# Optimization experiments

Measured on AMD Instinct MI355X. Metric: run time of the kernel, lower is better.

Reference implementation:

```python
import jax, jax.numpy as jnp
import numpy as np

N_NODES = 50000
TAU = 1.0 + (1.0 / 1000.0) * (0.1 - 1.0)  # anneal step 1 -> 0.9991


def setup_inputs() -> dict:
    key = jax.random.key(0)
    ks = jax.random.split(key, 8)
    N, F, H, E, K = N_NODES, 128, 128, 800000, 5
    node_features = jax.random.normal(ks[0], (N, F), dtype=jnp.float32)
    src = jnp.sort(jax.random.randint(ks[1], (E,), 0, N, dtype=jnp.int32))
    dst = jax.random.randint(ks[2], (E,), 0, N, dtype=jnp.int32)
    u_noise = jax.random.uniform(ks[3], (K, E), dtype=jnp.float32,
                                 minval=1e-6, maxval=1.0 - 1e-6)
    # MLP params: Linear(2F -> H), ReLU, Linear(H -> 1)
    W1 = jax.random.normal(ks[4], (2 * F, H), dtype=jnp.float32) / np.sqrt(2 * F)
    b1 = jnp.zeros((H,), dtype=jnp.float32)
    W2 = jax.random.normal(ks[5], (H, 1), dtype=jnp.float32) / np.sqrt(H)
    b2 = jnp.zeros((1,), dtype=jnp.float32)
    return {"node_features": node_features, "W1": W1, "b1": b1,
            "W2": W2, "b2": b2, "u_noise": u_noise, "src": src, "dst": dst}


def reference(node_features, W1, b1, W2, b2, u_noise, src, dst):
    N = N_NODES
    F = node_features.shape[1]
    # per-edge MLP on concat([x_u, x_v]) without materializing the (E, 2F) concat
    x_u = node_features[src]                      # (E, F)
    x_v = node_features[dst]                      # (E, F)
    h = jax.nn.relu(x_u @ W1[:F] + x_v @ W1[F:] + b1)   # (E, H)
    z = (h @ W2 + b2)[:, 0]                       # (E,)
    # per-node (segment) log-softmax over each node's neighbor edges
    zmax = jax.ops.segment_max(z, src, num_segments=N)
    ze = z - zmax[src]
    denom = jax.ops.segment_sum(jnp.exp(ze), src, num_segments=N)
    log_pi = ze - jnp.log(denom)[src]             # (E,)
    # k rounds of Gumbel-softmax sampling
    g = -jnp.log(-jnp.log(u_noise))               # (K, E)
    scores = (log_pi[None, :] + g) / TAU          # (K, E)

    def seg_softmax(s):
        m = jax.ops.segment_max(s, src, num_segments=N)
        e = jnp.exp(s - m[src])
        return e / jax.ops.segment_sum(e, src, num_segments=N)[src]

    def seg_argmax_dst(s):
        m = jax.ops.segment_max(s, src, num_segments=N)
        hit = s >= m[src]
        sel = jax.ops.segment_max(jnp.where(hit, dst, -1), src, num_segments=N)
        return sel  # (N,) selected neighbor per node, per round

    soft = jax.vmap(seg_softmax)(scores)          # (K, E) gumbel-softmax probs
    selected = jax.vmap(seg_argmax_dst)(scores)   # (K, N) sampled neighbor ids
    return selected, soft
```

## Files before the change

kernel.cpp:

```cpp
#include <hip/hip_runtime.h>

#define FEAT 128
#define HID  128
#define XS_S 132
#define MAXE 768
#define AS_S 132

__global__ __launch_bounds__(256) void gemm_ab(
    const float* __restrict__ X, const float* __restrict__ W1,
    const float* __restrict__ b1, float* __restrict__ A,
    float* __restrict__ B, int N) {
  __shared__ float xs[32 * XS_S];
  __shared__ float ws[32 * 64];
  const int t = threadIdx.x;
  const int n0 = blockIdx.x * 128;
  const int j0 = blockIdx.y * 64;
  const bool isA = j0 < 128;
  const float* Wbase = W1 + (isA ? j0 : 128 * HID + (j0 - 128));
  float* Obase = isA ? (A + j0) : (B + (j0 - 128));

  const int tn = t & 31;
  const int tc = t >> 5;

  float acc[4][8];
#pragma unroll
  for (int rr = 0; rr < 4; ++rr)
#pragma unroll
    for (int c = 0; c < 8; ++c) acc[rr][c] = 0.f;

  const int ln = t >> 3;
  const int lf = (t & 7) * 4;

  for (int kc = 0; kc < 4; ++kc) {
    __syncthreads();
#pragma unroll
    for (int rep = 0; rep < 4; ++rep) {
      const int nl = ln + rep * 32;
      const int n = n0 + nl;
      float4 v = make_float4(0.f, 0.f, 0.f, 0.f);
      if (n < N) v = *(const float4*)(X + (size_t)n * FEAT + kc * 32 + lf);
      xs[(lf + 0) * XS_S + nl] = v.x;
      xs[(lf + 1) * XS_S + nl] = v.y;
      xs[(lf + 2) * XS_S + nl] = v.z;
      xs[(lf + 3) * XS_S + nl] = v.w;
    }
#pragma unroll
    for (int rep = 0; rep < 2; ++rep) {
      const int idx = rep * 256 + t;
      const int wr = idx >> 4;
      const int c4 = (idx & 15) * 4;
      *(float4*)&ws[wr * 64 + c4] =
          *(const float4*)(Wbase + (size_t)(kc * 32 + wr) * HID + c4);
    }
    __syncthreads();

#pragma unroll 8
    for (int k = 0; k < 32; ++k) {
      const float4 xv = *(const float4*)&xs[k * XS_S + tn * 4];
      const float4 w0 = *(const float4*)&ws[k * 64 + tc * 8];
      const float4 w1 = *(const float4*)&ws[k * 64 + tc * 8 + 4];
      const float xr[4] = {xv.x, xv.y, xv.z, xv.w};
#pragma unroll
      for (int rr = 0; rr < 4; ++rr) {
        acc[rr][0] = fmaf(xr[rr], w0.x, acc[rr][0]);
        acc[rr][1] = fmaf(xr[rr], w0.y, acc[rr][1]);
        acc[rr][2] = fmaf(xr[rr], w0.z, acc[rr][2]);
        acc[rr][3] = fmaf(xr[rr], w0.w, acc[rr][3]);
        acc[rr][4] = fmaf(xr[rr], w1.x, acc[rr][4]);
        acc[rr][5] = fmaf(xr[rr], w1.y, acc[rr][5]);
        acc[rr][6] = fmaf(xr[rr], w1.z, acc[rr][6]);
        acc[rr][7] = fmaf(xr[rr], w1.w, acc[rr][7]);
      }
    }
  }

  float bb[8];
#pragma unroll
  for (int c = 0; c < 8; ++c) bb[c] = 0.f;
  if (isA) {
    *(float4*)&bb[0] = *(const float4*)(b1 + j0 + tc * 8);
    *(float4*)&bb[4] = *(const float4*)(b1 + j0 + tc * 8 + 4);
  }
#pragma unroll
  for (int rr = 0; rr < 4; ++rr) {
    const int n = n0 + tn * 4 + rr;
    if (n < N) {
      float* o = Obase + (size_t)n * HID + tc * 8;
      *(float4*)o = make_float4(acc[rr][0] + bb[0], acc[rr][1] + bb[1],
                                acc[rr][2] + bb[2], acc[rr][3] + bb[3]);
      *(float4*)(o + 4) = make_float4(acc[rr][4] + bb[4], acc[rr][5] + bb[5],
                                      acc[rr][6] + bb[6], acc[rr][7] + bb[7]);
    }
  }
}

__global__ __launch_bounds__(256) void fused_edge_seg(
    const float* __restrict__ A, const float* __restrict__ B,
    const float* __restrict__ W2, const float* __restrict__ b2,
    const int* __restrict__ src, const int* __restrict__ dst,
    const float* __restrict__ U, float* __restrict__ out_sel,
    float* __restrict__ out_soft, int N, int E, int K) {
  __shared__ float zs[MAXE];
  __shared__ int srcs[MAXE];
  __shared__ int dsts[MAXE];
  __shared__ float as[16 * AS_S];
  __shared__ int rsl[17];
  const int t = threadIdx.x;
  const int n0 = blockIdx.x * 16;
  const float INVTAU = 1.0f / 0.9991f;

  if (t < 17) {
    const int n = min(n0 + t, N);
    int lo = 0, hi = E;
    while (lo < hi) {
      const int mid = (lo + hi) >> 1;
      if (src[mid] < n) lo = mid + 1; else hi = mid;
    }
    rsl[t] = lo;
  }
#pragma unroll
  for (int rep = 0; rep < 2; ++rep) {
    const int idx = rep * 256 + t;
    const int row = idx >> 5;
    const int q4 = (idx & 31) * 4;
    const int gn = n0 + row;
    float4 v = make_float4(0.f, 0.f, 0.f, 0.f);
    if (gn < N) v = *(const float4*)(A + (size_t)gn * HID + q4);
    *(float4*)&as[row * AS_S + q4] = v;
  }
  __syncthreads();
  const int e_lo = rsl[0];
  const int cnt = min(rsl[16] - e_lo, MAXE);

  for (int i = t; i < cnt; i += 256) {
    srcs[i] = src[e_lo + i];
    dsts[i] = dst[e_lo + i];
  }
  __syncthreads();

  if (cnt > 0) {
    const int g2 = (t >> 4) * 2;
    const int l = t & 15;
    const float4 w0 = *(const float4*)(W2 + l * 8);
    const float4 w1 = *(const float4*)(W2 + l * 8 + 4);
    const float bias2 = b2[0];

#define LOADB(base_, B00, B01, B10, B11)                                      \
    {                                                                         \
      const int c0 = min((base_) + g2, cnt - 1);                              \
      const int c1 = min((base_) + g2 + 1, cnt - 1);                          \
      const float4* Bv0 = (const float4*)(B + (size_t)dsts[c0] * HID) + l * 2;\
      const float4* Bv1 = (const float4*)(B + (size_t)dsts[c1] * HID) + l * 2;\
      B00 = Bv0[0]; B01 = Bv0[1]; B10 = Bv1[0]; B11 = Bv1[1];                 \
    }

#define COMPUTE(base_, B00, B01, B10, B11)                                    \
    {                                                                         \
      const int i0 = (base_) + g2;                                            \
      const int c0 = min(i0, cnt - 1);                                        \
      const int c1 = min(i0 + 1, cnt - 1);                                    \
      const int u0 = srcs[c0] - n0;                                           \
      const int u1 = srcs[c1] - n0;                                           \
      const float4 a00 = *(const float4*)&as[u0 * AS_S + l * 8];              \
      const float4 a01 = *(const float4*)&as[u0 * AS_S + l * 8 + 4];          \
      const float4 a10 = *(const float4*)&as[u1 * AS_S + l * 8];              \
      const float4 a11 = *(const float4*)&as[u1 * AS_S + l * 8 + 4];          \
      float p0 = fmaxf(a00.x + B00.x, 0.f) * w0.x                             \
               + fmaxf(a00.y + B00.y, 0.f) * w0.y                             \
               + fmaxf(a00.z + B00.z, 0.f) * w0.z                             \
               + fmaxf(a00.w + B00.w, 0.f) * w0.w                             \
               + fmaxf(a01.x + B01.x, 0.f) * w1.x                             \
               + fmaxf(a01.y + B01.y, 0.f) * w1.y                             \
               + fmaxf(a01.z + B01.z, 0.f) * w1.z                             \
               + fmaxf(a01.w + B01.w, 0.f) * w1.w;                            \
      float p1 = fmaxf(a10.x + B10.x, 0.f) * w0.x                             \
               + fmaxf(a10.y + B10.y, 0.f) * w0.y                             \
               + fmaxf(a10.z + B10.z, 0.f) * w0.z                             \
               + fmaxf(a10.w + B10.w, 0.f) * w0.w                             \
               + fmaxf(a11.x + B11.x, 0.f) * w1.x                             \
               + fmaxf(a11.y + B11.y, 0.f) * w1.y                             \
               + fmaxf(a11.z + B11.z, 0.f) * w1.z                             \
               + fmaxf(a11.w + B11.w, 0.f) * w1.w;                            \
      _Pragma("unroll")                                                       \
      for (int m = 8; m >= 1; m >>= 1) {                                      \
        p0 += __shfl_xor(p0, m);                                              \
        p1 += __shfl_xor(p1, m);                                              \
      }                                                                       \
      if (l == 0) {                                                           \
        if (i0 < cnt) zs[i0] = p0 + bias2;                                    \
        if (i0 + 1 < cnt) zs[i0 + 1] = p1 + bias2;                            \
      }                                                                       \
    }

    float4 xb0, xb1, xb2, xb3;
    float4 yb0, yb1, yb2, yb3;
    LOADB(0, xb0, xb1, xb2, xb3)
    for (int base = 0; base < cnt; base += 64) {
      LOADB(base + 32, yb0, yb1, yb2, yb3)
      COMPUTE(base, xb0, xb1, xb2, xb3)
      LOADB(base + 64, xb0, xb1, xb2, xb3)
      COMPUTE(base + 32, yb0, yb1, yb2, yb3)
    }
#undef LOADB
#undef COMPUTE
  }
  __syncthreads();

  const int lane = t & 63;
  const int qtr = lane >> 4;
  const int ql = lane & 15;
  const int li = (t >> 6) * 4 + qtr;
  const int n = n0 + li;

  int start = 0, deg = 0;
  if (n < N) { start = rsl[li]; deg = rsl[li + 1] - start; }

  if (__all(deg <= 32)) {
    if (n >= N) return;
    if (deg == 0) {
      if (ql == 0)
        for (int k = 0; k < K; ++k) out_sel[(size_t)k * N + n] = -2147483648.0f;
      return;
    }
    const bool a0 = 2 * ql < deg;
    const bool a1 = 2 * ql + 1 < deg;
    const int le0 = start - e_lo + 2 * ql;
    const int le1 = le0 + 1;
    const int e0 = start + 2 * ql;
    const int e1 = e0 + 1;
    const float z0 = a0 ? zs[le0] : -INFINITY;
    const float z1 = a1 ? zs[le1] : -INFINITY;
    const int d0 = a0 ? dsts[le0] : -1;
    const int d1 = a1 ? dsts[le1] : -1;

    float zmax = fmaxf(z0, z1);
#pragma unroll
    for (int m = 8; m >= 1; m >>= 1) zmax = fmaxf(zmax, __shfl_xor(zmax, m));
    float den = (a0 ? __expf(z0 - zmax) : 0.f) + (a1 ? __expf(z1 - zmax) : 0.f);
#pragma unroll
    for (int m = 8; m >= 1; m >>= 1) den += __shfl_xor(den, m);
    const float logd = __logf(den);
    const float lp0 = (z0 - zmax) - logd;
    const float lp1 = (z1 - zmax) - logd;

    if (K == 5) {
      const size_t ce0 = (size_t)min(e0, E - 1);
      const size_t ce1 = (size_t)min(e1, E - 1);
      float u00, u01, u02, u03, u04, u10, u11, u12, u13, u14;
      u00 = U[0 * (size_t)E + ce0]; u10 = U[0 * (size_t)E + ce1];
      u01 = U[1 * (size_t)E + ce0]; u11 = U[1 * (size_t)E + ce1];
      u02 = U[2 * (size_t)E + ce0]; u12 = U[2 * (size_t)E + ce1];
      u03 = U[3 * (size_t)E + ce0]; u13 = U[3 * (size_t)E + ce1];
      u04 = U[4 * (size_t)E + ce0]; u14 = U[4 * (size_t)E + ce1];

#define GUMEX0(u) (a0 ? __expf((lp0 - __logf(-__logf(u))) * INVTAU) : 0.f)
#define GUMEX1(u) (a1 ? __expf((lp1 - __logf(-__logf(u))) * INVTAU) : 0.f)
      const float x00 = GUMEX0(u00), x10 = GUMEX1(u10);
      const float x01 = GUMEX0(u01), x11 = GUMEX1(u11);
      const float x02 = GUMEX0(u02), x12 = GUMEX1(u12);
      const float x03 = GUMEX0(u03), x13 = GUMEX1(u13);
      const float x04 = GUMEX0(u04), x14 = GUMEX1(u14);
#undef GUMEX0
#undef GUMEX1

#define ROUND(kk, ex0, ex1)                                                   \
      {                                                                       \
        float d2 = (ex0) + (ex1);                                             \
        float mx;                                                             \
        int md;                                                               \
        if ((ex1) > (ex0))      { mx = (ex1); md = d1; }                      \
        else if ((ex1) < (ex0)) { mx = (ex0); md = d0; }                      \
        else                    { mx = (ex0); md = max(d0, d1); }             \
        _Pragma("unroll")                                                     \
        for (int m = 8; m >= 1; m >>= 1) {                                    \
          d2 += __shfl_xor(d2, m);                                            \
          const float ox = __shfl_xor(mx, m);                                 \
          const int od = __shfl_xor(md, m);                                   \
          if (ox > mx) { mx = ox; md = od; }                                  \
          else if (ox == mx) md = max(md, od);                                \
        }                                                                     \
        if (ql == 0) out_sel[(size_t)(kk) * N + n] = (float)md;               \
        const float inv = __builtin_amdgcn_rcpf(d2);                          \
        if (a0) out_soft[(size_t)(kk) * E + e0] = (ex0) * inv;                \
        if (a1) out_soft[(size_t)(kk) * E + e1] = (ex1) * inv;                \
      }
      ROUND(0, x00, x10)
      ROUND(1, x01, x11)
      ROUND(2, x02, x12)
      ROUND(3, x03, x13)
      ROUND(4, x04, x14)
#undef ROUND
      return;
    }

    for (int k = 0; k < K; ++k) {
      float ex0 = 0.f, ex1 = 0.f;
      if (a0) {
        const float uu = U[(size_t)k * E + e0];
        const float gum = -__logf(-__logf(uu));
        ex0 = __expf((lp0 + gum) * INVTAU);
      }
      if (a1) {
        const float uu = U[(size_t)k * E + e1];
        const float gum = -__logf(-__logf(uu));
        ex1 = __expf((lp1 + gum) * INVTAU);
      }
      float d2 = ex0 + ex1;
      float mx;
      int md;
      if (ex1 > ex0)      { mx = ex1; md = d1; }
      else if (ex1 < ex0) { mx = ex0; md = d0; }
      else                { mx = ex0; md = max(d0, d1); }
#pragma unroll
      for (int m = 8; m >= 1; m >>= 1) {
        d2 += __shfl_xor(d2, m);
        const float ox = __shfl_xor(mx, m);
        const int od = __shfl_xor(md, m);
        if (ox > mx) { mx = ox; md = od; }
        else if (ox == mx) md = max(md, od);
      }
      if (ql == 0) out_sel[(size_t)k * N + n] = (float)md;
      const float inv = __builtin_amdgcn_rcpf(d2);
      if (a0) out_soft[(size_t)k * E + e0] = ex0 * inv;
      if (a1) out_soft[(size_t)k * E + e1] = ex1 * inv;
    }
    return;
  }

  const int lbase = (t >> 6) * 4;
  for (int j = 0; j < 4; ++j) {
    const int lj = lbase + j;
    const int nn = n0 + lj;
    if (nn >= N) continue;
    const int st = rsl[lj];
    const int dg = rsl[lj + 1] - st;
    const int lst = st - e_lo;
    if (dg == 0) {
      if (lane == 0)
        for (int k = 0; k < K; ++k) out_sel[(size_t)k * N + nn] = -2147483648.0f;
      continue;
    }
    float zmax = -INFINITY;
    for (int c = lane; c < dg; c += 64) zmax = fmaxf(zmax, zs[lst + c]);
#pragma unroll
    for (int m = 32; m >= 1; m >>= 1) zmax = fmaxf(zmax, __shfl_xor(zmax, m));
    float den = 0.f;
    for (int c = lane; c < dg; c += 64) den += expf(zs[lst + c] - zmax);
#pragma unroll
    for (int m = 32; m >= 1; m >>= 1) den += __shfl_xor(den, m);
    const float logd = logf(den);

    for (int k = 0; k < K; ++k) {
      float m2 = -INFINITY;
      for (int c = lane; c < dg; c += 64) {
        const float gum = -logf(-logf(U[(size_t)k * E + st + c]));
        const float s = ((zs[lst + c] - zmax) - logd + gum) * INVTAU;
        m2 = fmaxf(m2, s);
      }
#pragma unroll
      for (int m = 32; m >= 1; m >>= 1) m2 = fmaxf(m2, __shfl_xor(m2, m));
      float d2 = 0.f;
      int cand = -1;
      for (int c = lane; c < dg; c += 64) {
        const float gum = -logf(-logf(U[(size_t)k * E + st + c]));
        const float s = ((zs[lst + c] - zmax) - logd + gum) * INVTAU;
        d2 += expf(s - m2);
        if (s >= m2) cand = max(cand, dsts[lst + c]);
      }
#pragma unroll
      for (int m = 32; m >= 1; m >>= 1) d2 += __shfl_xor(d2, m);
#pragma unroll
      for (int m = 32; m >= 1; m >>= 1) cand = max(cand, __shfl_xor(cand, m));
      if (lane == 0) out_sel[(size_t)k * N + nn] = (float)cand;
      for (int c = lane; c < dg; c += 64) {
        const float gum = -logf(-logf(U[(size_t)k * E + st + c]));
        const float s = ((zs[lst + c] - zmax) - logd + gum) * INVTAU;
        out_soft[(size_t)k * E + st + c] = expf(s - m2) / d2;
      }
    }
  }
}

extern "C" void kernel_launch(void* const* d_in, const int* in_sizes, int n_in,
                              void* d_out, int out_size, void* d_ws, size_t ws_size,
                              hipStream_t stream) {
  const float* X  = (const float*)d_in[0];
  const float* W1 = (const float*)d_in[1];
  const float* b1 = (const float*)d_in[2];
  const float* W2 = (const float*)d_in[3];
  const float* b2 = (const float*)d_in[4];
  const float* U  = (const float*)d_in[5];
  const int* src  = (const int*)d_in[6];
  const int* dst  = (const int*)d_in[7];
  const int E = in_sizes[6];
  const int K = in_sizes[5] / E;
  const int N = in_sizes[0] / FEAT;

  float* A = (float*)d_ws;
  float* B = A + (size_t)N * HID;

  float* out_sel  = (float*)d_out;
  float* out_soft = (float*)d_out + (size_t)K * N;

  hipLaunchKernelGGL(gemm_ab, dim3((N + 127) / 128, 4), dim3(256), 0, stream,
                     X, W1, b1, A, B, N);
  hipLaunchKernelGGL(fused_edge_seg, dim3((N + 15) / 16), dim3(256), 0, stream,
                     A, B, W2, b2, src, dst, U, out_sel, out_soft, N, E, K);
}
```

Before: 232.1 us.

## Stage per-edge Gumbel exponentials in shared memory with block-wide coalesced passes

Replaces the per-node lane mapping, which used two edges per lane with a 64-lane fallback for high-degree nodes, with a uniform scheme. Log-probabilities are first written to shared memory. Then, for each round, all 256 threads compute exp-Gumbel values for the block's edge range with coalesced noise loads. Each 16-lane group then reduces its node's edges from shared memory to get the softmax sum and argmax. This removes the divergent fallback path and the uncoalesced noise reads, but adds block barriers per round and reuses shared buffers (srcs, as) as scratch.

```diff
diff --git a/kernel.cpp b/kernel.cpp
--- a/kernel.cpp
+++ b/kernel.cpp
@@ -206,6 +206,9 @@
   }
   __syncthreads();
 
+  float* lps = (float*)srcs;
+  float* exs = as;
+
   const int lane = t & 63;
   const int qtr = lane >> 4;
   const int ql = lane & 15;
@@ -214,170 +217,55 @@
 
   int start = 0, deg = 0;
   if (n < N) { start = rsl[li]; deg = rsl[li + 1] - start; }
-
-  if (__all(deg <= 32)) {
-    if (n >= N) return;
-    if (deg == 0) {
-      if (ql == 0)
-        for (int k = 0; k < K; ++k) out_sel[(size_t)k * N + n] = -2147483648.0f;
-      return;
-    }
-    const bool a0 = 2 * ql < deg;
-    const bool a1 = 2 * ql + 1 < deg;
-    const int le0 = start - e_lo + 2 * ql;
-    const int le1 = le0 + 1;
-    const int e0 = start + 2 * ql;
-    const int e1 = e0 + 1;
-    const float z0 = a0 ? zs[le0] : -INFINITY;
-    const float z1 = a1 ? zs[le1] : -INFINITY;
-    const int d0 = a0 ? dsts[le0] : -1;
-    const int d1 = a1 ? dsts[le1] : -1;
-
-    float zmax = fmaxf(z0, z1);
+  const int lst = start - e_lo;
+
+  {
+    float zmax = -INFINITY;
+    for (int c = ql; c < deg; c += 16) zmax = fmaxf(zmax, zs[lst + c]);
 #pragma unroll
     for (int m = 8; m >= 1; m >>= 1) zmax = fmaxf(zmax, __shfl_xor(zmax, m));
-    float den = (a0 ? __expf(z0 - zmax) : 0.f) + (a1 ? __expf(z1 - zmax) : 0.f);
+    float den = 0.f;
+    for (int c = ql; c < deg; c += 16) den += __expf(zs[lst + c] - zmax);
 #pragma unroll
     for (int m = 8; m >= 1; m >>= 1) den += __shfl_xor(den, m);
     const float logd = __logf(den);
-    const float lp0 = (z0 - zmax) - logd;
-    const float lp1 = (z1 - zmax) - logd;
-
-    if (K == 5) {
-      const size_t ce0 = (size_t)min(e0, E - 1);
-      const size_t ce1 = (size_t)min(e1, E - 1);
-      float u00, u01, u02, u03, u04, u10, u11, u12, u13, u14;
-      u00 = U[0 * (size_t)E + ce0]; u10 = U[0 * (size_t)E + ce1];
-      u01 = U[1 * (size_t)E + ce0]; u11 = U[1 * (size_t)E + ce1];
-      u02 = U[2 * (size_t)E + ce0]; u12 = U[2 * (size_t)E + ce1];
-      u03 = U[3 * (size_t)E + ce0]; u13 = U[3 * (size_t)E + ce1];
-      u04 = U[4 * (size_t)E + ce0]; u14 = U[4 * (size_t)E + ce1];
-
-#define GUMEX0(u) (a0 ? __expf((lp0 - __logf(-__logf(u))) * INVTAU) : 0.f)
-#define GUMEX1(u) (a1 ? __expf((lp1 - __logf(-__logf(u))) * INVTAU) : 0.f)
-      const float x00 = GUMEX0(u00), x10 = GUMEX1(u10);
-      const float x01 = GUMEX0(u01), x11 = GUMEX1(u11);
-      const float x02 = GUMEX0(u02), x12 = GUMEX1(u12);
-      const float x03 = GUMEX0(u03), x13 = GUMEX1(u13);
-      const float x04 = GUMEX0(u04), x14 = GUMEX1(u14);
-#undef GUMEX0
-#undef GUMEX1
-
-#define ROUND(kk, ex0, ex1)                                                   \
-      {                                                                       \
-        float d2 = (ex0) + (ex1);                                             \
-        float mx;                                                             \
-        int md;                                                               \
-        if ((ex1) > (ex0))      { mx = (ex1); md = d1; }                      \
-        else if ((ex1) < (ex0)) { mx = (ex0); md = d0; }                      \
-        else                    { mx = (ex0); md = max(d0, d1); }             \
-        _Pragma("unroll")                                                     \
-        for (int m = 8; m >= 1; m >>= 1) {                                    \
-          d2 += __shfl_xor(d2, m);                                            \
-          const float ox = __shfl_xor(mx, m);                                 \
-          const int od = __shfl_xor(md, m);                                   \
-          if (ox > mx) { mx = ox; md = od; }                                  \
-          else if (ox == mx) md = max(md, od);                                \
-        }                                                                     \
-        if (ql == 0) out_sel[(size_t)(kk) * N + n] = (float)md;               \
-        const float inv = __builtin_amdgcn_rcpf(d2);                          \
-        if (a0) out_soft[(size_t)(kk) * E + e0] = (ex0) * inv;                \
-        if (a1) out_soft[(size_t)(kk) * E + e1] = (ex1) * inv;                \
-      }
-      ROUND(0, x00, x10)
-      ROUND(1, x01, x11)
-      ROUND(2, x02, x12)
-      ROUND(3, x03, x13)
-      ROUND(4, x04, x14)
-#undef ROUND
-      return;
-    }
-
-    for (int k = 0; k < K; ++k) {
-      float ex0 = 0.f, ex1 = 0.f;
-      if (a0) {
-        const float uu = U[(size_t)k * E + e0];
-        const float gum = -__logf(-__logf(uu));
-        ex0 = __expf((lp0 + gum) * INVTAU);
-      }
-      if (a1) {
-        const float uu = U[(size_t)k * E + e1];
-        const float gum = -__logf(-__logf(uu));
-        ex1 = __expf((lp1 + gum) * INVTAU);
-      }
-      float d2 = ex0 + ex1;
-      float mx;
-      int md;
-      if (ex1 > ex0)      { mx = ex1; md = d1; }
-      else if (ex1 < ex0) { mx = ex0; md = d0; }
-      else                { mx = ex0; md = max(d0, d1); }
-#pragma unroll
-      for (int m = 8; m >= 1; m >>= 1) {
-        d2 += __shfl_xor(d2, m);
-        const float ox = __shfl_xor(mx, m);
-        const int od = __shfl_xor(md, m);
-        if (ox > mx) { mx = ox; md = od; }
-        else if (ox == mx) md = max(md, od);
-      }
-      if (ql == 0) out_sel[(size_t)k * N + n] = (float)md;
-      const float inv = __builtin_amdgcn_rcpf(d2);
-      if (a0) out_soft[(size_t)k * E + e0] = ex0 * inv;
-      if (a1) out_soft[(size_t)k * E + e1] = ex1 * inv;
-    }
-    return;
-  }
-
-  const int lbase = (t >> 6) * 4;
-  for (int j = 0; j < 4; ++j) {
-    const int lj = lbase + j;
-    const int nn = n0 + lj;
-    if (nn >= N) continue;
-    const int st = rsl[lj];
-    const int dg = rsl[lj + 1] - st;
-    const int lst = st - e_lo;
-    if (dg == 0) {
-      if (lane == 0)
-        for (int k = 0; k < K; ++k) out_sel[(size_t)k * N + nn] = -2147483648.0f;
-      continue;
-    }
-    float zmax = -INFINITY;
-    for (int c = lane; c < dg; c += 64) zmax = fmaxf(zmax, zs[lst + c]);
-#pragma unroll
-    for (int m = 32; m >= 1; m >>= 1) zmax = fmaxf(zmax, __shfl_xor(zmax, m));
-    float den = 0.f;
-    for (int c = lane; c < dg; c += 64) den += expf(zs[lst + c] - zmax);
-#pragma unroll
-    for (int m = 32; m >= 1; m >>= 1) den += __shfl_xor(den, m);
-    const float logd = logf(den);
-
-    for (int k = 0; k < K; ++k) {
-      float m2 = -INFINITY;
-      for (int c = lane; c < dg; c += 64) {
-        const float gum = -logf(-logf(U[(size_t)k * E + st + c]));
-        const float s = ((zs[lst + c] - zmax) - logd + gum) * INVTAU;
-        m2 = fmaxf(m2, s);
-      }
-#pragma unroll
-      for (int m = 32; m >= 1; m >>= 1) m2 = fmaxf(m2, __shfl_xor(m2, m));
-      float d2 = 0.f;
-      int cand = -1;
-      for (int c = lane; c < dg; c += 64) {
-        const float gum = -logf(-logf(U[(size_t)k * E + st + c]));
-        const float s = ((zs[lst + c] - zmax) - logd + gum) * INVTAU;
-        d2 += expf(s - m2);
-        if (s >= m2) cand = max(cand, dsts[lst + c]);
-      }
-#pragma unroll
-      for (int m = 32; m >= 1; m >>= 1) d2 += __shfl_xor(d2, m);
-#pragma unroll
-      for (int m = 32; m >= 1; m >>= 1) cand = max(cand, __shfl_xor(cand, m));
-      if (lane == 0) out_sel[(size_t)k * N + nn] = (float)cand;
-      for (int c = lane; c < dg; c += 64) {
-        const float gum = -logf(-logf(U[(size_t)k * E + st + c]));
-        const float s = ((zs[lst + c] - zmax) - logd + gum) * INVTAU;
-        out_soft[(size_t)k * E + st + c] = expf(s - m2) / d2;
-      }
-    }
+    for (int c = ql; c < deg; c += 16)
+      lps[lst + c] = (zs[lst + c] - zmax) - logd;
+  }
+  __syncthreads();
+
+  for (int k = 0; k < K; ++k) {
+    const size_t ub = (size_t)k * E + e_lo;
+    for (int i = t; i < cnt; i += 256) {
+      const float uu = U[ub + i];
+      exs[i] = __expf((lps[i] - __logf(-__logf(uu))) * INVTAU);
+    }
+    __syncthreads();
+
+    float d2 = 0.f, mx = -INFINITY;
+    int md = -1;
+    for (int c = ql; c < deg; c += 16) {
+      const float ex = exs[lst + c];
+      d2 += ex;
+      const int dd = dsts[lst + c];
+      if (ex > mx) { mx = ex; md = dd; }
+      else if (ex == mx) md = max(md, dd);
+    }
+#pragma unroll
+    for (int m = 8; m >= 1; m >>= 1) {
+      d2 += __shfl_xor(d2, m);
+      const float ox = __shfl_xor(mx, m);
+      const int od = __shfl_xor(md, m);
+      if (ox > mx) { mx = ox; md = od; }
+      else if (ox == mx) md = max(md, od);
+    }
+    if (n < N && ql == 0)
+      out_sel[(size_t)k * N + n] =
+          (deg > 0) ? (float)md : -2147483648.0f;
+    const float inv = __builtin_amdgcn_rcpf(d2);
+    for (int c = ql; c < deg; c += 16)
+      out_soft[(size_t)k * E + start + c] = exs[lst + c] * inv;
+    __syncthreads();
   }
 }
 
```

Measured after the change: 219.2 us. 1.06x faster.
